# Kernel optimization log

Hardware: AMD Instinct MI355X
Metric: run time of the kernel (lower is better)

Reference implementation:

```python
import jax, jax.numpy as jnp
import numpy as np

NEG_INF = -1e30  # masked_softmax fill (squad util convention)


def setup_inputs() -> dict:
    key = jax.random.key(0)
    ks = jax.random.split(key, 5)
    B, S, H = 4, 2048, 512
    x = jax.random.normal(ks[0], (B, S, H), dtype=jnp.float32)
    mask = jax.random.randint(ks[1], (B, S), 0, 2, dtype=jnp.int32)
    mask = mask.at[:, 0].set(1)  # ensure at least one valid key per row
    W_comb = jax.random.normal(ks[2], (H, 3 * H), dtype=jnp.float32) * (1.0 / np.sqrt(H))
    b_comb = jnp.zeros((3 * H,), dtype=jnp.float32)
    W_out = jax.random.normal(ks[3], (H, H), dtype=jnp.float32) * (1.0 / np.sqrt(H))
    b_out = jnp.zeros((H,), dtype=jnp.float32)
    return {"x": x, "mask": mask, "W_comb": W_comb, "b_comb": b_comb,
            "W_out": W_out, "b_out": b_out}


def reference(x, mask, W_comb, b_comb, W_out, b_out):
    B, S, H = x.shape
    n_head = 8
    d = H // n_head
    scale = d ** 0.5
    qkv = x @ W_comb + b_comb                      # [B,S,3H]
    q, k, v = jnp.split(qkv, 3, axis=-1)
    q = q.reshape(B, S, n_head, d)
    k = k.reshape(B, S, n_head, d)
    v = v.reshape(B, S, n_head, d)
    # [B,h,Sq,Sk] scores; mask applies along the key axis
    scores = jnp.einsum('bqhd,bkhd->bhqk', q / scale, k)
    key_mask = (mask > 0)[:, None, None, :]        # [B,1,1,Sk]
    logits = jnp.where(key_mask, scores, NEG_INF)
    attn = jax.nn.softmax(logits, axis=-1)         # dropout = identity (eval)
    out = jnp.einsum('bhqk,bkhd->bqhd', attn, v).reshape(B, S, H)
    return out @ W_out + b_out
```

## Files before the change

### kernel.cpp

```cpp
#include <hip/hip_runtime.h>
#include <hip/hip_bf16.h>
#include <stdint.h>

typedef unsigned short u16;
typedef unsigned int u32;
typedef __attribute__((ext_vector_type(8))) __bf16 bf16x8;
typedef __attribute__((ext_vector_type(8))) unsigned short us8;
typedef __attribute__((ext_vector_type(4))) unsigned short us4;
typedef __attribute__((ext_vector_type(4))) float f32x4;
typedef __attribute__((ext_vector_type(16))) float f32x16;
typedef __attribute__((ext_vector_type(4))) unsigned int u32x4;
typedef __attribute__((ext_vector_type(2))) unsigned int u32x2;

#define KSCALE_Q 0.18033688011112042f

__device__ inline u16 f2bf(float f) {
  union { __bf16 b; u16 s; } x; x.b = (__bf16)f; return x.s;
}
__device__ inline u32 packbf(float a, float b) {
  return (u32)f2bf(a) | ((u32)f2bf(b) << 16);
}
__device__ inline f32x16 zero16() {
  f32x16 z; for (int i = 0; i < 16; ++i) z[i] = 0.f; return z;
}
__device__ __forceinline__ void gl_lds16(const u16* g, u16* l) {
  __builtin_amdgcn_global_load_lds(
      (const __attribute__((address_space(1))) void*)g,
      (__attribute__((address_space(3))) void*)l, 16, 0, 0);
}
__device__ __forceinline__ void pl32swap(u32& a, u32& b) {
#if __has_builtin(__builtin_amdgcn_permlane32_swap)
  u32x2 r = __builtin_amdgcn_permlane32_swap(a, b, false, false);
  a = r[0]; b = r[1];
#else
  u32 ta = (u32)__shfl_xor((int)a, 32);
  u32 tb = (u32)__shfl_xor((int)b, 32);
  int hi = (threadIdx.x & 63) >> 5;
  u32 na = hi ? tb : a;
  u32 nb = hi ? b : ta;
  a = na; b = nb;
#endif
}

__global__ __launch_bounds__(256) void prep(
    const float* __restrict__ x, const float* __restrict__ Wc,
    const float* __restrict__ Wo, const int* __restrict__ mask,
    u16* __restrict__ xbf, u16* __restrict__ wct, u16* __restrict__ wot,
    int* __restrict__ idx, int* __restrict__ nbv) {
  int r = blockIdx.x, tid = threadIdx.x;
  if (r < 4096) {
    int i = r * 256 + tid;
    float4 v = ((const float4*)x)[i];
    us4 o;
    o[0] = f2bf(v.x); o[1] = f2bf(v.y); o[2] = f2bf(v.z); o[3] = f2bf(v.w);
    ((us4*)xbf)[i] = o;
    return;
  }
  __shared__ float tile[32][33];
  __shared__ int ps[256];
  if (r < 5120) {
    const float* in; u16* outT; int R, C, bi;
    if (r < 4864) { in = Wc; outT = wct; R = 512; C = 1536; bi = r - 4096; }
    else          { in = Wo; outT = wot; R = 512; C = 512;  bi = r - 4864; }
    int nbx = C >> 5;
    int bx = bi % nbx, by = bi / nbx;
    int xq = tid & 31, yq = tid >> 5;
    int c0 = bx * 32, r0 = by * 32;
    for (int j = 0; j < 32; j += 8)
      tile[yq + j][xq] = in[(size_t)(r0 + yq + j) * C + c0 + xq];
    __syncthreads();
    for (int j = 0; j < 32; j += 8)
      outT[(size_t)(c0 + yq + j) * R + r0 + xq] = f2bf(tile[xq][yq + j]);
    return;
  }
  int b = r - 5120;
  const int* mrow = mask + b * 2048;
  int4 a = ((const int4*)mrow)[tid * 2];
  int4 c = ((const int4*)mrow)[tid * 2 + 1];
  int v[8] = {a.x, a.y, a.z, a.w, c.x, c.y, c.z, c.w};
  int cnt = 0;
  for (int i = 0; i < 8; ++i) cnt += (v[i] > 0);
  ps[tid] = cnt;
  __syncthreads();
  for (int off = 1; off < 256; off <<= 1) {
    int xv = ps[tid];
    int yv = (tid >= off) ? ps[tid - off] : 0;
    __syncthreads();
    ps[tid] = xv + yv;
    __syncthreads();
  }
  int total = ps[255];
  int pos = ps[tid] - cnt;
  int* ip = idx + b * 2048;
  for (int i = 0; i < 8; ++i)
    if (v[i] > 0) ip[pos++] = tid * 8 + i;
  for (int i = 0; i < 8; ++i) {
    int j = tid * 8 + i;
    if (j >= total) ip[j] = 0;
  }
  if (tid == 0) nbv[b] = total;
}

__global__ __launch_bounds__(256) void gemm_qkv(
    const u16* __restrict__ A, const u16* __restrict__ Bt,
    const float* __restrict__ bias, u16* __restrict__ Qc,
    u16* __restrict__ Kc, u16* __restrict__ VTc,
    const int* __restrict__ idx, const int* __restrict__ nbv) {
  const int K = 512;
  int bid = blockIdx.x;
  bool isQ = bid < 256;
  int b = 0, m0, n0;
  if (isQ) {
    m0 = (bid >> 2) * 128;
    n0 = (bid & 3) * 128;
  } else {
    int t = bid - 256;
    b = t >> 7;
    int rr_ = t & 127;
    m0 = (rr_ & 15) * 128;
    n0 = (rr_ >> 4) * 128 + 512;
    int npad = (nbv[b] + 127) & ~127;
    if (m0 >= npad) return;
  }
  __shared__ __align__(16) u16 As[128 * 64];
  __shared__ __align__(16) u16 Bs[128 * 64];
  int tid = threadIdx.x, wave = tid >> 6, lane = tid & 63;
  int quad = lane >> 4, l16 = lane & 15;
  int wm = (wave >> 1) * 64, wn = (wave & 1) * 64;

  int r8 = lane >> 3;
  int cb = (lane & 7) ^ r8;
  const u16* agp[4];
  for (int i = 0; i < 4; ++i) {
    int row = m0 + wave * 32 + i * 8 + r8;
    int grow = isQ ? row : (b * 2048 + idx[b * 2048 + row]);
    agp[i] = A + (size_t)grow * K + cb * 8;
  }
  const u16* bg = Bt + (size_t)(n0 + wave * 32 + r8) * K + cb * 8;
  u16* al = As + (wave * 32) * 64 + lane * 8;
  u16* bl = Bs + (wave * 32) * 64 + lane * 8;

  f32x4 acc[4][4];
  for (int i = 0; i < 4; ++i)
    for (int j = 0; j < 4; ++j) acc[i][j] = (f32x4){0.f, 0.f, 0.f, 0.f};

  int rx = l16 & 7;
  for (int kk = 0; kk < K; kk += 64) {
    __syncthreads();
    for (int i = 0; i < 4; ++i)
      gl_lds16(agp[i] + kk, al + i * 8 * 64);
    for (int i = 0; i < 4; ++i)
      gl_lds16(bg + kk + (size_t)(i * 8) * K, bl + i * 8 * 64);
    __syncthreads();
    for (int ks = 0; ks < 2; ++ks) {
      int pos = ((ks * 4 + quad) ^ rx) * 8;
      bf16x8 af[4], bfr[4];
      for (int i = 0; i < 4; ++i)
        af[i] = *(const bf16x8*)(As + (wm + i * 16 + l16) * 64 + pos);
      for (int j = 0; j < 4; ++j)
        bfr[j] = *(const bf16x8*)(Bs + (wn + j * 16 + l16) * 64 + pos);
      for (int i = 0; i < 4; ++i)
        for (int j = 0; j < 4; ++j)
          acc[i][j] = __builtin_amdgcn_mfma_f32_16x16x32_bf16(
              af[i], bfr[j], acc[i][j], 0, 0, 0);
    }
  }
  for (int j = 0; j < 4; ++j) {
    int col = n0 + wn + j * 16 + l16;
    float bv = bias[col];
    if (isQ) {
      for (int i = 0; i < 4; ++i) {
        int rowb = m0 + wm + i * 16 + quad * 4;
        for (int rr = 0; rr < 4; ++rr)
          Qc[(size_t)(rowb + rr) * 512 + col] =
              f2bf((acc[i][j][rr] + bv) * KSCALE_Q);
      }
    } else if (col < 1024) {
      int ck = col - 512;
      for (int i = 0; i < 4; ++i) {
        int key0 = m0 + wm + i * 16 + quad * 4;
        for (int rr = 0; rr < 4; ++rr)
          Kc[((size_t)b * 2048 + key0 + rr) * 512 + ck] =
              f2bf(acc[i][j][rr] + bv);
      }
    } else {
      int hd = col - 1024;
      int h = hd >> 6, d = hd & 63;
      u16* vrow = VTc + ((size_t)(b * 8 + h) * 64 + d) * 2048;
      for (int i = 0; i < 4; ++i) {
        int key0 = m0 + wm + i * 16 + quad * 4;
        us4 pk;
        for (int rr = 0; rr < 4; ++rr) pk[rr] = f2bf(acc[i][j][rr] + bv);
        *(us4*)(vrow + key0) = pk;
      }
    }
  }
}

__global__ __launch_bounds__(256) void gemm_out(
    const u16* __restrict__ A, const u16* __restrict__ Bt,
    const float* __restrict__ bias, float* __restrict__ Cout) {
  const int K = 512, N = 512;
  int m0 = blockIdx.y * 128, n0 = blockIdx.x * 128;
  __shared__ __align__(16) u16 As[128 * 64];
  __shared__ __align__(16) u16 Bs[128 * 64];
  int tid = threadIdx.x, wave = tid >> 6, lane = tid & 63;
  int quad = lane >> 4, l16 = lane & 15;
  int wm = (wave >> 1) * 64, wn = (wave & 1) * 64;

  int r8 = lane >> 3;
  int cb = (lane & 7) ^ r8;
  const u16* ag = A + (size_t)(m0 + wave * 32 + r8) * K + cb * 8;
  const u16* bg = Bt + (size_t)(n0 + wave * 32 + r8) * K + cb * 8;
  u16* al = As + (wave * 32) * 64 + lane * 8;
  u16* bl = Bs + (wave * 32) * 64 + lane * 8;

  f32x4 acc[4][4];
  for (int i = 0; i < 4; ++i)
    for (int j = 0; j < 4; ++j) acc[i][j] = (f32x4){0.f, 0.f, 0.f, 0.f};

  int rx = l16 & 7;
  for (int kk = 0; kk < K; kk += 64) {
    __syncthreads();
    for (int i = 0; i < 4; ++i)
      gl_lds16(ag + kk + (size_t)(i * 8) * K, al + i * 8 * 64);
    for (int i = 0; i < 4; ++i)
      gl_lds16(bg + kk + (size_t)(i * 8) * K, bl + i * 8 * 64);
    __syncthreads();
    for (int ks = 0; ks < 2; ++ks) {
      int pos = ((ks * 4 + quad) ^ rx) * 8;
      bf16x8 af[4], bfr[4];
      for (int i = 0; i < 4; ++i)
        af[i] = *(const bf16x8*)(As + (wm + i * 16 + l16) * 64 + pos);
      for (int j = 0; j < 4; ++j)
        bfr[j] = *(const bf16x8*)(Bs + (wn + j * 16 + l16) * 64 + pos);
      for (int i = 0; i < 4; ++i)
        for (int j = 0; j < 4; ++j)
          acc[i][j] = __builtin_amdgcn_mfma_f32_16x16x32_bf16(
              af[i], bfr[j], acc[i][j], 0, 0, 0);
    }
  }
  for (int j = 0; j < 4; ++j) {
    int col = n0 + wn + j * 16 + l16;
    float bv = bias[col];
    for (int i = 0; i < 4; ++i) {
      int rowb = m0 + wm + i * 16 + quad * 4;
      for (int rr = 0; rr < 4; ++rr)
        Cout[(size_t)(rowb + rr) * N + col] = acc[i][j][rr] + bv;
    }
  }
}

__global__ __launch_bounds__(256) void attn_kernel(
    const u16* __restrict__ Qc, const u16* __restrict__ Kc,
    const u16* __restrict__ VTc, const int* __restrict__ nbv,
    u16* __restrict__ aout) {
  int b = blockIdx.z, h = blockIdx.y, q0 = blockIdx.x * 256;
  int bh = b * 8 + h;
  int tid = threadIdx.x, wave = tid >> 6, lane = tid & 63;
  int l5 = lane & 31, hi = lane >> 5;
  int nb = nbv[b];
  int npad = (nb + 127) & ~127;

  __shared__ __align__(16) u16 Kt[128 * 64];
  __shared__ __align__(16) u16 Vt[64 * 128];

  bf16x8 qf[2][4];
  for (int qg = 0; qg < 2; ++qg) {
    int qrow = b * 2048 + q0 + wave * 64 + qg * 32 + l5;
    for (int s = 0; s < 4; ++s)
      qf[qg][s] = *(const bf16x8*)(Qc + (size_t)qrow * 512 + h * 64 + s * 16 +
                                   hi * 8);
  }

  f32x16 o[2][2];
  for (int qg = 0; qg < 2; ++qg)
    for (int dc = 0; dc < 2; ++dc) o[qg][dc] = zero16();
  float lsum[2] = {0.f, 0.f};

  int krr = lane >> 3;
  int kcb = (lane & 7) ^ krr;
  const u16* kg = Kc + ((size_t)(b * 2048) + wave * 32 + krr) * 512 + h * 64 +
                  kcb * 8;
  u16* kl = Kt + (wave * 32) * 64 + lane * 8;
  int vrr = lane >> 4;
  u16* vl = Vt + (wave * 16) * 128 + lane * 8;

  for (int kt0 = 0; kt0 < npad; kt0 += 128) {
    __syncthreads();
    for (int i = 0; i < 4; ++i)
      gl_lds16(kg + (size_t)(kt0 + i * 8) * 512, kl + i * 8 * 64);
    for (int i = 0; i < 4; ++i) {
      int vr = wave * 16 + i * 4 + vrr;
      int vcb = (lane & 15) ^ (vr & 15);
      gl_lds16(VTc + ((size_t)(bh * 64) + vr) * 2048 + kt0 + vcb * 8,
               vl + i * 4 * 128);
    }
    __syncthreads();

    for (int kg4 = 0; kg4 < 4; ++kg4) {
      int krow = kg4 * 32 + l5;
      const u16* kro = Kt + krow * 64;
      int rx = krow & 7;
      bf16x8 ka[4];
      for (int s = 0; s < 4; ++s)
        ka[s] = *(const bf16x8*)(kro + ((s * 2 + hi) ^ rx) * 8);
      bf16x8 pb[2][2];
      for (int qg = 0; qg < 2; ++qg) {
        f32x16 sa = zero16();
        for (int s = 0; s < 4; ++s)
          sa = __builtin_amdgcn_mfma_f32_32x32x16_bf16(ka[s], qf[qg][s], sa,
                                                       0, 0, 0);
        if (kt0 + 128 > nb) {
          for (int r = 0; r < 16; ++r) {
            int jg = kt0 + kg4 * 32 + (r & 3) + 8 * (r >> 2) + 4 * hi;
            if (jg >= nb) sa[r] = -1e30f;
          }
        }
        u32 pk[8];
        float ls = 0.f;
        for (int j = 0; j < 8; ++j) {
          float e0 = __builtin_amdgcn_exp2f(sa[2 * j]);
          float e1 = __builtin_amdgcn_exp2f(sa[2 * j + 1]);
          ls += e0 + e1;
          pk[j] = packbf(e0, e1);
        }
        lsum[qg] += ls;
        for (int t = 0; t < 2; ++t) {
          u32 a0 = pk[t * 4 + 0], a2 = pk[t * 4 + 2];
          u32 a1 = pk[t * 4 + 1], a3 = pk[t * 4 + 3];
          pl32swap(a0, a2);
          pl32swap(a1, a3);
          u32x4 qv; qv[0] = a0; qv[1] = a1; qv[2] = a2; qv[3] = a3;
          pb[qg][t] = __builtin_bit_cast(bf16x8, qv);
        }
      }
      for (int t = 0; t < 2; ++t) {
        int cblk = kg4 * 4 + t * 2 + hi;
        for (int dc = 0; dc < 2; ++dc) {
          int vrow = dc * 32 + l5;
          bf16x8 va = *(const bf16x8*)(Vt + vrow * 128 +
                                       ((cblk ^ (vrow & 15)) * 8));
          for (int qg = 0; qg < 2; ++qg)
            o[qg][dc] = __builtin_amdgcn_mfma_f32_32x32x16_bf16(
                va, pb[qg][t], o[qg][dc], 0, 0, 0);
        }
      }
    }
  }

  for (int qg = 0; qg < 2; ++qg) {
    float lt = lsum[qg];
    lt += __shfl_xor(lt, 32);
    float inv = 1.f / lt;
    int qrow = b * 2048 + q0 + wave * 64 + qg * 32 + l5;
    for (int dc = 0; dc < 2; ++dc)
      for (int mI = 0; mI < 4; ++mI) {
        us4 pk;
        for (int r = 0; r < 4; ++r) pk[r] = f2bf(o[qg][dc][mI * 4 + r] * inv);
        *(us4*)(aout + (size_t)qrow * 512 + h * 64 + dc * 32 + mI * 8 +
                hi * 4) = pk;
      }
  }
}

extern "C" void kernel_launch(void* const* d_in, const int* in_sizes, int n_in,
                              void* d_out, int out_size, void* d_ws,
                              size_t ws_size, hipStream_t stream) {
  const float* x = (const float*)d_in[0];
  const int* mask = (const int*)d_in[1];
  const float* Wc = (const float*)d_in[2];
  const float* bc = (const float*)d_in[3];
  const float* Wo = (const float*)d_in[4];
  const float* bo = (const float*)d_in[5];
  float* out = (float*)d_out;

  char* ws = (char*)d_ws;
  u16* xbf = (u16*)(ws);
  u16* wct = (u16*)(ws + 8388608);
  u16* wot = (u16*)(ws + 9961472);
  u16* Qc  = (u16*)(ws + 10485760);
  u16* Kc  = (u16*)(ws + 18874368);
  u16* vtc = (u16*)(ws + 27262976);
  int* idx = (int*)(ws + 35651584);
  int* nbv = (int*)(ws + 35684352);
  u16* aout = xbf;

  prep<<<5124, 256, 0, stream>>>(x, Wc, Wo, mask, xbf, wct, wot, idx, nbv);
  gemm_qkv<<<768, 256, 0, stream>>>(xbf, wct, bc, Qc, Kc, vtc, idx, nbv);
  attn_kernel<<<dim3(8, 8, 4), 256, 0, stream>>>(Qc, Kc, vtc, nbv, aout);
  gemm_out<<<dim3(4, 64), 256, 0, stream>>>(aout, wot, bo, out);
}
```

Baseline: 156.3 us.

## Double-buffer LDS tiles with async prefetch in GEMM and attention kernels

Converts the QKV GEMM, output GEMM and attention kernels to double-buffered shared memory. The next K/V or A/B tile is issued with global_load_lds before computing on the current one, and explicit vmcnt waits plus raw barriers replace the paired __syncthreads. This overlaps global-to-LDS transfer latency with MFMA work. It also interleaves the two query-group score MFMAs and adds unroll pragmas. The cost is twice the LDS per block, which may lower occupancy, and the hand-placed vmcnt counts depend on the exact number of loads issued per thread.

Measured after the change: 152.4 us. 1.03x faster.

```diff
diff --git a/kernel.cpp b/kernel.cpp
--- a/kernel.cpp
+++ b/kernel.cpp
@@ -13,6 +13,9 @@
 typedef __attribute__((ext_vector_type(2))) unsigned int u32x2;
 
 #define KSCALE_Q 0.18033688011112042f
+
+#define VMCNT(n) asm volatile("s_waitcnt vmcnt(" #n ")" ::: "memory")
+#define BARRIER() __builtin_amdgcn_s_barrier()
 
 __device__ inline u16 f2bf(float f) {
   union { __bf16 b; u16 s; } x; x.b = (__bf16)f; return x.s;
@@ -122,8 +125,8 @@
     int npad = (nbv[b] + 127) & ~127;
     if (m0 >= npad) return;
   }
-  __shared__ __align__(16) u16 As[128 * 64];
-  __shared__ __align__(16) u16 Bs[128 * 64];
+  __shared__ __align__(16) u16 As[2][128 * 64];
+  __shared__ __align__(16) u16 Bs[2][128 * 64];
   int tid = threadIdx.x, wave = tid >> 6, lane = tid & 63;
   int quad = lane >> 4, l16 = lane & 15;
   int wm = (wave >> 1) * 64, wn = (wave & 1) * 64;
@@ -137,33 +140,50 @@
     agp[i] = A + (size_t)grow * K + cb * 8;
   }
   const u16* bg = Bt + (size_t)(n0 + wave * 32 + r8) * K + cb * 8;
-  u16* al = As + (wave * 32) * 64 + lane * 8;
-  u16* bl = Bs + (wave * 32) * 64 + lane * 8;
+  int lofs = (wave * 32) * 64 + lane * 8;
 
   f32x4 acc[4][4];
   for (int i = 0; i < 4; ++i)
     for (int j = 0; j < 4; ++j) acc[i][j] = (f32x4){0.f, 0.f, 0.f, 0.f};
 
   int rx = l16 & 7;
-  for (int kk = 0; kk < K; kk += 64) {
-    __syncthreads();
+
+  auto stage = [&](int buf, int kk) {
+    u16* al = As[buf] + lofs;
+    u16* bl = Bs[buf] + lofs;
+#pragma unroll
     for (int i = 0; i < 4; ++i)
       gl_lds16(agp[i] + kk, al + i * 8 * 64);
+#pragma unroll
     for (int i = 0; i < 4; ++i)
       gl_lds16(bg + kk + (size_t)(i * 8) * K, bl + i * 8 * 64);
-    __syncthreads();
+  };
+
+  stage(0, 0);
+  for (int t = 0; t < 8; ++t) {
+    if (t < 7) { stage((t + 1) & 1, (t + 1) * 64); VMCNT(8); }
+    else       { VMCNT(0); }
+    BARRIER();
+    const u16* Asb = As[t & 1];
+    const u16* Bsb = Bs[t & 1];
+#pragma unroll
     for (int ks = 0; ks < 2; ++ks) {
       int pos = ((ks * 4 + quad) ^ rx) * 8;
       bf16x8 af[4], bfr[4];
+#pragma unroll
       for (int i = 0; i < 4; ++i)
-        af[i] = *(const bf16x8*)(As + (wm + i * 16 + l16) * 64 + pos);
+        af[i] = *(const bf16x8*)(Asb + (wm + i * 16 + l16) * 64 + pos);
+#pragma unroll
       for (int j = 0; j < 4; ++j)
-        bfr[j] = *(const bf16x8*)(Bs + (wn + j * 16 + l16) * 64 + pos);
+        bfr[j] = *(const bf16x8*)(Bsb + (wn + j * 16 + l16) * 64 + pos);
+#pragma unroll
       for (int i = 0; i < 4; ++i)
+#pragma unroll
         for (int j = 0; j < 4; ++j)
           acc[i][j] = __builtin_amdgcn_mfma_f32_16x16x32_bf16(
               af[i], bfr[j], acc[i][j], 0, 0, 0);
     }
+    BARRIER();
   }
   for (int j = 0; j < 4; ++j) {
     int col = n0 + wn + j * 16 + l16;
@@ -202,8 +222,8 @@
     const float* __restrict__ bias, float* __restrict__ Cout) {
   const int K = 512, N = 512;
   int m0 = blockIdx.y * 128, n0 = blockIdx.x * 128;
-  __shared__ __align__(16) u16 As[128 * 64];
-  __shared__ __align__(16) u16 Bs[128 * 64];
+  __shared__ __align__(16) u16 As[2][128 * 64];
+  __shared__ __align__(16) u16 Bs[2][128 * 64];
   int tid = threadIdx.x, wave = tid >> 6, lane = tid & 63;
   int quad = lane >> 4, l16 = lane & 15;
   int wm = (wave >> 1) * 64, wn = (wave & 1) * 64;
@@ -212,33 +232,50 @@
   int cb = (lane & 7) ^ r8;
   const u16* ag = A + (size_t)(m0 + wave * 32 + r8) * K + cb * 8;
   const u16* bg = Bt + (size_t)(n0 + wave * 32 + r8) * K + cb * 8;
-  u16* al = As + (wave * 32) * 64 + lane * 8;
-  u16* bl = Bs + (wave * 32) * 64 + lane * 8;
+  int lofs = (wave * 32) * 64 + lane * 8;
 
   f32x4 acc[4][4];
   for (int i = 0; i < 4; ++i)
     for (int j = 0; j < 4; ++j) acc[i][j] = (f32x4){0.f, 0.f, 0.f, 0.f};
 
   int rx = l16 & 7;
-  for (int kk = 0; kk < K; kk += 64) {
-    __syncthreads();
+
+  auto stage = [&](int buf, int kk) {
+    u16* al = As[buf] + lofs;
+    u16* bl = Bs[buf] + lofs;
+#pragma unroll
     for (int i = 0; i < 4; ++i)
       gl_lds16(ag + kk + (size_t)(i * 8) * K, al + i * 8 * 64);
+#pragma unroll
     for (int i = 0; i < 4; ++i)
       gl_lds16(bg + kk + (size_t)(i * 8) * K, bl + i * 8 * 64);
-    __syncthreads();
+  };
+
+  stage(0, 0);
+  for (int t = 0; t < 8; ++t) {
+    if (t < 7) { stage((t + 1) & 1, (t + 1) * 64); VMCNT(8); }
+    else       { VMCNT(0); }
+    BARRIER();
+    const u16* Asb = As[t & 1];
+    const u16* Bsb = Bs[t & 1];
+#pragma unroll
     for (int ks = 0; ks < 2; ++ks) {
       int pos = ((ks * 4 + quad) ^ rx) * 8;
       bf16x8 af[4], bfr[4];
+#pragma unroll
       for (int i = 0; i < 4; ++i)
-        af[i] = *(const bf16x8*)(As + (wm + i * 16 + l16) * 64 + pos);
+        af[i] = *(const bf16x8*)(Asb + (wm + i * 16 + l16) * 64 + pos);
+#pragma unroll
       for (int j = 0; j < 4; ++j)
-        bfr[j] = *(const bf16x8*)(Bs + (wn + j * 16 + l16) * 64 + pos);
+        bfr[j] = *(const bf16x8*)(Bsb + (wn + j * 16 + l16) * 64 + pos);
+#pragma unroll
       for (int i = 0; i < 4; ++i)
+#pragma unroll
         for (int j = 0; j < 4; ++j)
           acc[i][j] = __builtin_amdgcn_mfma_f32_16x16x32_bf16(
               af[i], bfr[j], acc[i][j], 0, 0, 0);
     }
+    BARRIER();
   }
   for (int j = 0; j < 4; ++j) {
     int col = n0 + wn + j * 16 + l16;
@@ -261,20 +298,26 @@
   int l5 = lane & 31, hi = lane >> 5;
   int nb = nbv[b];
   int npad = (nb + 127) & ~127;
-
-  __shared__ __align__(16) u16 Kt[128 * 64];
-  __shared__ __align__(16) u16 Vt[64 * 128];
+  int NT = npad >> 7;
+
+  __shared__ __align__(16) u16 Kt[2][128 * 64];
+  __shared__ __align__(16) u16 Vt[2][64 * 128];
 
   bf16x8 qf[2][4];
+#pragma unroll
   for (int qg = 0; qg < 2; ++qg) {
     int qrow = b * 2048 + q0 + wave * 64 + qg * 32 + l5;
+#pragma unroll
     for (int s = 0; s < 4; ++s)
       qf[qg][s] = *(const bf16x8*)(Qc + (size_t)qrow * 512 + h * 64 + s * 16 +
                                    hi * 8);
   }
+  VMCNT(0);
 
   f32x16 o[2][2];
+#pragma unroll
   for (int qg = 0; qg < 2; ++qg)
+#pragma unroll
     for (int dc = 0; dc < 2; ++dc) o[qg][dc] = zero16();
   float lsum[2] = {0.f, 0.f};
 
@@ -282,79 +325,108 @@
   int kcb = (lane & 7) ^ krr;
   const u16* kg = Kc + ((size_t)(b * 2048) + wave * 32 + krr) * 512 + h * 64 +
                   kcb * 8;
-  u16* kl = Kt + (wave * 32) * 64 + lane * 8;
   int vrr = lane >> 4;
-  u16* vl = Vt + (wave * 16) * 128 + lane * 8;
-
-  for (int kt0 = 0; kt0 < npad; kt0 += 128) {
-    __syncthreads();
+
+  auto stageKV = [&](int buf, int kt0) {
+    u16* kl = Kt[buf] + (wave * 32) * 64 + lane * 8;
+#pragma unroll
     for (int i = 0; i < 4; ++i)
       gl_lds16(kg + (size_t)(kt0 + i * 8) * 512, kl + i * 8 * 64);
+    u16* vl = Vt[buf] + (wave * 16) * 128 + lane * 8;
+#pragma unroll
     for (int i = 0; i < 4; ++i) {
       int vr = wave * 16 + i * 4 + vrr;
       int vcb = (lane & 15) ^ (vr & 15);
       gl_lds16(VTc + ((size_t)(bh * 64) + vr) * 2048 + kt0 + vcb * 8,
                vl + i * 4 * 128);
     }
-    __syncthreads();
-
+  };
+
+  stageKV(0, 0);
+  for (int t = 0; t < NT; ++t) {
+    if (t + 1 < NT) { stageKV((t + 1) & 1, (t + 1) * 128); VMCNT(8); }
+    else            { VMCNT(0); }
+    BARRIER();
+    const u16* Ktc = Kt[t & 1];
+    const u16* Vtc = Vt[t & 1];
+    int kt0 = t * 128;
+    bool maskT = (kt0 + 128 > nb);
+
+#pragma unroll
     for (int kg4 = 0; kg4 < 4; ++kg4) {
       int krow = kg4 * 32 + l5;
-      const u16* kro = Kt + krow * 64;
+      const u16* kro = Ktc + krow * 64;
       int rx = krow & 7;
       bf16x8 ka[4];
+#pragma unroll
       for (int s = 0; s < 4; ++s)
         ka[s] = *(const bf16x8*)(kro + ((s * 2 + hi) ^ rx) * 8);
+      f32x16 sa[2];
+      sa[0] = zero16(); sa[1] = zero16();
+#pragma unroll
+      for (int s = 0; s < 4; ++s) {
+        sa[0] = __builtin_amdgcn_mfma_f32_32x32x16_bf16(ka[s], qf[0][s],
+                                                        sa[0], 0, 0, 0);
+        sa[1] = __builtin_amdgcn_mfma_f32_32x32x16_bf16(ka[s], qf[1][s],
+                                                        sa[1], 0, 0, 0);
+      }
       bf16x8 pb[2][2];
+#pragma unroll
       for (int qg = 0; qg < 2; ++qg) {
-        f32x16 sa = zero16();
-        for (int s = 0; s < 4; ++s)
-          sa = __builtin_amdgcn_mfma_f32_32x32x16_bf16(ka[s], qf[qg][s], sa,
-                                                       0, 0, 0);
-        if (kt0 + 128 > nb) {
+        if (maskT) {
+#pragma unroll
           for (int r = 0; r < 16; ++r) {
             int jg = kt0 + kg4 * 32 + (r & 3) + 8 * (r >> 2) + 4 * hi;
-            if (jg >= nb) sa[r] = -1e30f;
+            if (jg >= nb) sa[qg][r] = -1e30f;
           }
         }
         u32 pk[8];
         float ls = 0.f;
+#pragma unroll
         for (int j = 0; j < 8; ++j) {
-          float e0 = __builtin_amdgcn_exp2f(sa[2 * j]);
-          float e1 = __builtin_amdgcn_exp2f(sa[2 * j + 1]);
+          float e0 = __builtin_amdgcn_exp2f(sa[qg][2 * j]);
+          float e1 = __builtin_amdgcn_exp2f(sa[qg][2 * j + 1]);
           ls += e0 + e1;
           pk[j] = packbf(e0, e1);
         }
         lsum[qg] += ls;
-        for (int t = 0; t < 2; ++t) {
-          u32 a0 = pk[t * 4 + 0], a2 = pk[t * 4 + 2];
-          u32 a1 = pk[t * 4 + 1], a3 = pk[t * 4 + 3];
+#pragma unroll
+        for (int t2 = 0; t2 < 2; ++t2) {
+          u32 a0 = pk[t2 * 4 + 0], a2 = pk[t2 * 4 + 2];
+          u32 a1 = pk[t2 * 4 + 1], a3 = pk[t2 * 4 + 3];
           pl32swap(a0, a2);
           pl32swap(a1, a3);
           u32x4 qv; qv[0] = a0; qv[1] = a1; qv[2] = a2; qv[3] = a3;
-          pb[qg][t] = __builtin_bit_cast(bf16x8, qv);
+          pb[qg][t2] = __builtin_bit_cast(bf16x8, qv);
         }
       }
-      for (int t = 0; t < 2; ++t) {
-        int cblk = kg4 * 4 + t * 2 + hi;
+#pragma unroll
+      for (int t2 = 0; t2 < 2; ++t2) {
+        int cblk = kg4 * 4 + t2 * 2 + hi;
+#pragma unroll
         for (int dc = 0; dc < 2; ++dc) {
           int vrow = dc * 32 + l5;
-          bf16x8 va = *(const bf16x8*)(Vt + vrow * 128 +
+          bf16x8 va = *(const bf16x8*)(Vtc + vrow * 128 +
                                        ((cblk ^ (vrow & 15)) * 8));
-          for (int qg = 0; qg < 2; ++qg)
-            o[qg][dc] = __builtin_amdgcn_mfma_f32_32x32x16_bf16(
-                va, pb[qg][t], o[qg][dc], 0, 0, 0);
+          o[0][dc] = __builtin_amdgcn_mfma_f32_32x32x16_bf16(
+              va, pb[0][t2], o[0][dc], 0, 0, 0);
+          o[1][dc] = __builtin_amdgcn_mfma_f32_32x32x16_bf16(
+              va, pb[1][t2], o[1][dc], 0, 0, 0);
         }
       }
     }
-  }
-
+    BARRIER();
+  }
+
+#pragma unroll
   for (int qg = 0; qg < 2; ++qg) {
     float lt = lsum[qg];
     lt += __shfl_xor(lt, 32);
     float inv = 1.f / lt;
     int qrow = b * 2048 + q0 + wave * 64 + qg * 32 + l5;
+#pragma unroll
     for (int dc = 0; dc < 2; ++dc)
+#pragma unroll
       for (int mI = 0; mI < 4; ++mI) {
         us4 pk;
         for (int r = 0; r < 4; ++r) pk[r] = f2bf(o[qg][dc][mI * 4 + r] * inv);
```
